# Performance work log

Hardware: AMD Instinct MI355X
Metric: run time of the kernel (lower is better)

The kernel has to match this reference:

```python
import jax, jax.numpy as jnp
import numpy as np

H = 50  # hidden_size


def _lstm_layer(x, W_ih, W_hh, b_ih, b_hh):
    """Single LSTM layer, batch_first input x: [B, T, D] -> [B, T, H].
    PyTorch gate order in the 4H dim: i, f, g, o."""
    B, T, D = x.shape
    # Precompute input projections for all timesteps: [T, B, 4H]
    x_proj = jnp.einsum('btd,gd->tbg', x, W_ih) + (b_ih + b_hh)

    def step(carry, xt):
        h, c = carry
        gates = xt + h @ W_hh.T  # [B, 4H]
        i, f, g, o = jnp.split(gates, 4, axis=-1)
        i = jax.nn.sigmoid(i)
        f = jax.nn.sigmoid(f)
        g = jnp.tanh(g)
        o = jax.nn.sigmoid(o)
        c = f * c + i * g
        h = o * jnp.tanh(c)
        return (h, c), h

    h0 = jnp.zeros((B, H), dtype=x.dtype)
    c0 = jnp.zeros((B, H), dtype=x.dtype)
    _, hs = jax.lax.scan(step, (h0, c0), x_proj)  # hs: [T, B, H]
    return jnp.transpose(hs, (1, 0, 2))  # [B, T, H]


def setup_inputs() -> dict:
    key = jax.random.key(0)
    ks = jax.random.split(key, 11)
    B, T = 2048, 512
    s = 1.0 / np.sqrt(H)  # PyTorch uniform init bound
    u = lambda k, shape: jax.random.uniform(k, shape, jnp.float32, -s, s)
    return {
        'x': jax.random.normal(ks[0], (B, T, 1), dtype=jnp.float32),
        'W_ih0': u(ks[1], (4 * H, 1)),
        'W_hh0': u(ks[2], (4 * H, H)),
        'b_ih0': u(ks[3], (4 * H,)),
        'b_hh0': u(ks[4], (4 * H,)),
        'W_ih1': u(ks[5], (4 * H, H)),
        'W_hh1': u(ks[6], (4 * H, H)),
        'b_ih1': u(ks[7], (4 * H,)),
        'b_hh1': u(ks[8], (4 * H,)),
        'W_fc': u(ks[9], (1, H)),
        'b_fc': u(ks[10], (1,)),
    }


def reference(x, W_ih0, W_hh0, b_ih0, b_hh0, W_ih1, W_hh1, b_ih1, b_hh1, W_fc, b_fc):
    out = _lstm_layer(x, W_ih0, W_hh0, b_ih0, b_hh0)     # [B, T, H]
    out = _lstm_layer(out, W_ih1, W_hh1, b_ih1, b_hh1)   # [B, T, H]
    return out[:, -1, :] @ W_fc.T + b_fc                  # [B, 1]
```

## Files before the change

### kernel.cpp

```cpp
#include <hip/hip_runtime.h>

#define TT   512
#define HH   50
#define MB   8
#define NW   13
#define NTHR (NW * 64)
#define BUFH 2560

typedef _Float16 f16x8 __attribute__((ext_vector_type(8)));
typedef float    f32x4 __attribute__((ext_vector_type(4)));

#define L2E 1.4426950408889634f

__device__ __forceinline__ float rcp_f(float v) { return __builtin_amdgcn_rcpf(v); }
__device__ __forceinline__ float ex2_f(float v) { return __builtin_amdgcn_exp2f(v); }

__global__ __launch_bounds__(NTHR, 1)
void lstm2_kernel(const float* __restrict__ x,
                  const float* __restrict__ W_ih0, const float* __restrict__ W_hh0,
                  const float* __restrict__ b_ih0, const float* __restrict__ b_hh0,
                  const float* __restrict__ W_ih1, const float* __restrict__ W_hh1,
                  const float* __restrict__ b_ih1, const float* __restrict__ b_hh1,
                  const float* __restrict__ W_fc,  const float* __restrict__ b_fc,
                  float* __restrict__ out)
{
    __shared__ __align__(16) _Float16 shh[2][BUFH];
    __shared__ float sh_x[MB][TT + 4];
    __shared__ float shf[MB][52];
    __shared__ float sh_wfc[HH];

    const int tid = threadIdx.x;
    const int w   = tid >> 6;
    const int l   = tid & 63;
    const int q   = l >> 4;
    const int n   = l & 15;
    const int b0  = blockIdx.x * MB;

    for (int i = tid; i < 2 * BUFH; i += NTHR) (&shh[0][0])[i] = (_Float16)0.0f;
    for (int i = tid; i < MB * TT; i += NTHR)
        sh_x[i >> 9][i & (TT - 1)] = x[(size_t)b0 * TT + i];
    for (int i = tid; i < HH; i += NTHR) sh_wfc[i] = W_fc[i];

    const int  u_r   = w * 4 + (n >> 2);
    const bool rowok = (u_r < HH);
    const int  grow  = (n & 3) * HH + (rowok ? u_r : 0);
    const float srow = ((n & 3) == 2) ? (2.0f * L2E) : (-L2E);

    f16x8 wf[5];
    #pragma unroll
    for (int ki = 0; ki < 5; ++ki) {
        #pragma unroll
        for (int e = 0; e < 8; ++e) {
            int k = ki * 32 + q * 8 + e;
            float v = 0.0f;
            if (rowok) {
                if      (k < HH)           v = W_hh0[grow * HH + k];
                else if (k < 2 * HH)       v = W_ih1[grow * HH + (k - HH)];
                else if (k < 3 * HH)       v = W_hh1[grow * HH + (k - 2 * HH)];
            }
            wf[ki][e] = (_Float16)(srow * v);
        }
    }

    const bool isL1 = (n >= 8);
    const int  u    = 4 * w + q;
    const int  cb   = n & 7;
    const bool wr   = (u < HH);
    const int  uc   = wr ? u : 0;

    float bz[4], wz[4];
    #pragma unroll
    for (int e = 0; e < 4; ++e) {
        int gr = e * HH + uc;
        float sc = (e == 2) ? (2.0f * L2E) : (-L2E);
        bz[e] = sc * (isL1 ? (b_ih1[gr] + b_hh1[gr]) : (b_ih0[gr] + b_hh0[gr]));
        wz[e] = isL1 ? 0.0f : (sc * W_ih0[gr]);
    }

    auto offrc = [](int r, int c) {
        return (r >> 5) * 512 + ((r >> 3) & 3) * 128 + c * 8 + (r & 7);
    };
    const _Float16* rb = &shh[0][8 * l];
    const int oa = isL1 ? offrc(100 + uc, cb + 8) : offrc(uc, cb);
    const int ob = offrc(50 + uc, cb + 8);
    _Float16* wpa0 = &shh[1][oa];
    _Float16* wpa1 = &shh[0][oa];
    _Float16* wpb0 = &shh[1][ob];
    _Float16* wpb1 = &shh[0][ob];

    const float* xq = &sh_x[cb][0];
    float cst = 0.0f;

    __syncthreads();

#define MFMA(A, B, C) __builtin_amdgcn_mfma_f32_16x16x32_f16((A), (B), (C), 0, 0, 0)

#define STEP(P, T0, XI)                                                           \
    {                                                                             \
        float xi = (XI);                                                          \
        f32x4 cin;                                                                \
        cin[0] = __builtin_fmaf(xi, wz[0], bz[0]);                                \
        cin[1] = __builtin_fmaf(xi, wz[1], bz[1]);                                \
        cin[2] = __builtin_fmaf(xi, wz[2], bz[2]);                                \
        cin[3] = __builtin_fmaf(xi, wz[3], bz[3]);                                \
        f16x8 b0 = *(const f16x8*)(rb + (P) * BUFH);                              \
        f16x8 b1 = *(const f16x8*)(rb + (P) * BUFH + 512);                        \
        f16x8 b2 = *(const f16x8*)(rb + (P) * BUFH + 1024);                       \
        f16x8 b3 = *(const f16x8*)(rb + (P) * BUFH + 1536);                       \
        f16x8 b4 = *(const f16x8*)(rb + (P) * BUFH + 2048);                       \
        f32x4 a = MFMA(wf[0], b0, cin);                                           \
        a = MFMA(wf[1], b1, a);                                                   \
        a = MFMA(wf[2], b2, a);                                                   \
        a = MFMA(wf[3], b3, a);                                                   \
        a = MFMA(wf[4], b4, a);                                                   \
        float eI = ex2_f(a[0]), eF = ex2_f(a[1]), tG = ex2_f(a[2]), eO = ex2_f(a[3]); \
        float dI = 1.0f + eI, dF = 1.0f + eF, dO = 1.0f + eO;                     \
        float IG = (tG - 1.0f) * rcp_f(dI * (tG + 1.0f));                         \
        float cn = __builtin_fmaf(rcp_f(dF), cst, IG);                            \
        cst = ((T0) && isL1) ? 0.0f : cn;                                         \
        float cc = __builtin_amdgcn_fmed3f(cst, -16.0f, 16.0f);                   \
        float tc = ex2_f(cc * (2.0f * L2E));                                      \
        float hv = (tc - 1.0f) * rcp_f(dO * (tc + 1.0f));                         \
        if (wr && !((T0) && isL1)) {                                              \
            _Float16 h16 = (_Float16)hv;                                          \
            *((P) ? wpa1 : wpa0) = h16;                                           \
            if (!isL1) *((P) ? wpb1 : wpb0) = h16;                                \
        }                                                                         \
        __syncthreads();                                                          \
    }

    STEP(0, 1, xq[0])
    for (int k2 = 0; k2 < 255; ++k2) {
        STEP(1, 0, xq[1])
        STEP(0, 0, xq[2])
        xq += 2;
    }
    STEP(1, 0, xq[1])
#undef STEP

    {
        f32x4 cin = {bz[0], bz[1], bz[2], bz[3]};
        f16x8 b0 = *(const f16x8*)(rb);
        f16x8 b1 = *(const f16x8*)(rb + 512);
        f16x8 b2 = *(const f16x8*)(rb + 1024);
        f16x8 b3 = *(const f16x8*)(rb + 1536);
        f16x8 b4 = *(const f16x8*)(rb + 2048);
        f32x4 a = MFMA(wf[0], b0, cin);
        a = MFMA(wf[1], b1, a);
        a = MFMA(wf[2], b2, a);
        a = MFMA(wf[3], b3, a);
        a = MFMA(wf[4], b4, a);
        if (isL1 && wr) {
            float eI = ex2_f(a[0]), eF = ex2_f(a[1]), tG = ex2_f(a[2]), eO = ex2_f(a[3]);
            float dI = 1.0f + eI, dF = 1.0f + eF, dO = 1.0f + eO;
            float IG = (tG - 1.0f) * rcp_f(dI * (tG + 1.0f));
            float cn = __builtin_fmaf(rcp_f(dF), cst, IG);
            float cc = __builtin_amdgcn_fmed3f(cn, -16.0f, 16.0f);
            float tc = ex2_f(cc * (2.0f * L2E));
            shf[cb][uc] = (tc - 1.0f) * rcp_f(dO * (tc + 1.0f));
        }
    }
    __syncthreads();

    if (tid < MB) {
        float s = b_fc[0];
        for (int j = 0; j < HH; ++j) s += shf[tid][j] * sh_wfc[j];
        out[b0 + tid] = s;
    }
#undef MFMA
}

extern "C" void kernel_launch(void* const* d_in, const int* in_sizes, int n_in,
                              void* d_out, int out_size, void* d_ws, size_t ws_size,
                              hipStream_t stream) {
    const float* xin   = (const float*)d_in[0];
    const float* W_ih0 = (const float*)d_in[1];
    const float* W_hh0 = (const float*)d_in[2];
    const float* b_ih0 = (const float*)d_in[3];
    const float* b_hh0 = (const float*)d_in[4];
    const float* W_ih1 = (const float*)d_in[5];
    const float* W_hh1 = (const float*)d_in[6];
    const float* b_ih1 = (const float*)d_in[7];
    const float* b_hh1 = (const float*)d_in[8];
    const float* W_fc  = (const float*)d_in[9];
    const float* b_fc  = (const float*)d_in[10];
    float* out = (float*)d_out;

    lstm2_kernel<<<dim3(2048 / MB), dim3(NTHR), 0, stream>>>(
        xin, W_ih0, W_hh0, b_ih0, b_hh0, W_ih1, W_hh1, b_ih1, b_hh1, W_fc, b_fc, out);
}
```

Before: 240.6 us.

## Halve wavefronts per block, each wave computing two hidden-unit tiles

Cuts the block from 13 wavefronts to 7, with each wave holding two sets of weight fragments and running two interleaved MFMA chains per timestep, covering 8 hidden units instead of 4. This makes the per-step __syncthreads cheaper and reuses the loaded B operands across two MFMA chains. Interleaving the two independent accumulation chains can hide MFMA latency. The cost is more register pressure and twice the gate math per wave on the serial critical path.

```diff
diff --git a/kernel.cpp b/kernel.cpp
--- a/kernel.cpp
+++ b/kernel.cpp
@@ -3,7 +3,7 @@
 #define TT   512
 #define HH   50
 #define MB   8
-#define NW   13
+#define NW   7
 #define NTHR (NW * 64)
 #define BUFH 2560
 
@@ -26,7 +26,7 @@
 {
     __shared__ __align__(16) _Float16 shh[2][BUFH];
     __shared__ float sh_x[MB][TT + 4];
-    __shared__ float shf[MB][52];
+    __shared__ float shf[MB][56];
     __shared__ float sh_wfc[HH];
 
     const int tid = threadIdx.x;
@@ -41,90 +41,122 @@
         sh_x[i >> 9][i & (TT - 1)] = x[(size_t)b0 * TT + i];
     for (int i = tid; i < HH; i += NTHR) sh_wfc[i] = W_fc[i];
 
-    const int  u_r   = w * 4 + (n >> 2);
-    const bool rowok = (u_r < HH);
-    const int  grow  = (n & 3) * HH + (rowok ? u_r : 0);
     const float srow = ((n & 3) == 2) ? (2.0f * L2E) : (-L2E);
-
-    f16x8 wf[5];
-    #pragma unroll
-    for (int ki = 0; ki < 5; ++ki) {
-        #pragma unroll
-        for (int e = 0; e < 8; ++e) {
-            int k = ki * 32 + q * 8 + e;
-            float v = 0.0f;
-            if (rowok) {
-                if      (k < HH)           v = W_hh0[grow * HH + k];
-                else if (k < 2 * HH)       v = W_ih1[grow * HH + (k - HH)];
-                else if (k < 3 * HH)       v = W_hh1[grow * HH + (k - 2 * HH)];
-            }
-            wf[ki][e] = (_Float16)(srow * v);
-        }
-    }
+    f16x8 wf0[5], wf1[5];
+
+#define LOADW(WF, TOFF)                                                           \
+    {                                                                             \
+        int ur   = 8 * w + (TOFF) + (n >> 2);                                     \
+        bool rok = (ur < HH);                                                     \
+        int grow = (n & 3) * HH + (rok ? ur : 0);                                 \
+        _Pragma("unroll")                                                         \
+        for (int ki = 0; ki < 5; ++ki) {                                          \
+            _Pragma("unroll")                                                     \
+            for (int e = 0; e < 8; ++e) {                                         \
+                int k = ki * 32 + q * 8 + e;                                      \
+                float v = 0.0f;                                                   \
+                if (rok) {                                                        \
+                    if      (k < HH)      v = W_hh0[grow * HH + k];               \
+                    else if (k < 2 * HH)  v = W_ih1[grow * HH + (k - HH)];        \
+                    else if (k < 3 * HH)  v = W_hh1[grow * HH + (k - 2 * HH)];    \
+                }                                                                 \
+                WF[ki][e] = (_Float16)(srow * v);                                 \
+            }                                                                     \
+        }                                                                         \
+    }
+    LOADW(wf0, 0)
+    LOADW(wf1, 4)
+#undef LOADW
 
     const bool isL1 = (n >= 8);
-    const int  u    = 4 * w + q;
     const int  cb   = n & 7;
-    const bool wr   = (u < HH);
-    const int  uc   = wr ? u : 0;
-
-    float bz[4], wz[4];
+    const int  u0   = 8 * w + q,      u1 = u0 + 4;
+    const bool wr0  = (u0 < HH),      wr1 = (u1 < HH);
+    const int  uc0  = wr0 ? u0 : 0;
+    const int  uc1  = wr1 ? u1 : 0;
+
+    float bz0[4], wz0[4], bz1[4], wz1[4];
     #pragma unroll
     for (int e = 0; e < 4; ++e) {
-        int gr = e * HH + uc;
         float sc = (e == 2) ? (2.0f * L2E) : (-L2E);
-        bz[e] = sc * (isL1 ? (b_ih1[gr] + b_hh1[gr]) : (b_ih0[gr] + b_hh0[gr]));
-        wz[e] = isL1 ? 0.0f : (sc * W_ih0[gr]);
+        int g0 = e * HH + uc0, g1 = e * HH + uc1;
+        bz0[e] = sc * (isL1 ? (b_ih1[g0] + b_hh1[g0]) : (b_ih0[g0] + b_hh0[g0]));
+        bz1[e] = sc * (isL1 ? (b_ih1[g1] + b_hh1[g1]) : (b_ih0[g1] + b_hh0[g1]));
+        wz0[e] = isL1 ? 0.0f : (sc * W_ih0[g0]);
+        wz1[e] = isL1 ? 0.0f : (sc * W_ih0[g1]);
     }
 
     auto offrc = [](int r, int c) {
         return (r >> 5) * 512 + ((r >> 3) & 3) * 128 + c * 8 + (r & 7);
     };
     const _Float16* rb = &shh[0][8 * l];
-    const int oa = isL1 ? offrc(100 + uc, cb + 8) : offrc(uc, cb);
-    const int ob = offrc(50 + uc, cb + 8);
-    _Float16* wpa0 = &shh[1][oa];
-    _Float16* wpa1 = &shh[0][oa];
-    _Float16* wpb0 = &shh[1][ob];
-    _Float16* wpb1 = &shh[0][ob];
+    const int oa0 = isL1 ? offrc(100 + uc0, cb + 8) : offrc(uc0, cb);
+    const int ob0 = offrc(50 + uc0, cb + 8);
+    const int oa1 = isL1 ? offrc(100 + uc1, cb + 8) : offrc(uc1, cb);
+    const int ob1 = offrc(50 + uc1, cb + 8);
 
     const float* xq = &sh_x[cb][0];
-    float cst = 0.0f;
+    float cst0 = 0.0f, cst1 = 0.0f;
 
     __syncthreads();
 
 #define MFMA(A, B, C) __builtin_amdgcn_mfma_f32_16x16x32_f16((A), (B), (C), 0, 0, 0)
+
+#define CHAIN(ACC, CST, T0, HV)                                                   \
+    {                                                                             \
+        float eI = ex2_f(ACC[0]), eF = ex2_f(ACC[1]);                             \
+        float tG = ex2_f(ACC[2]), eO = ex2_f(ACC[3]);                             \
+        float dI = 1.0f + eI, dF = 1.0f + eF, dO = 1.0f + eO;                     \
+        float IG = (tG - 1.0f) * rcp_f(dI * (tG + 1.0f));                         \
+        float cn = __builtin_fmaf(rcp_f(dF), CST, IG);                            \
+        CST = ((T0) && isL1) ? 0.0f : cn;                                         \
+        float cc = __builtin_amdgcn_fmed3f(CST, -16.0f, 16.0f);                   \
+        float tc = ex2_f(cc * (2.0f * L2E));                                      \
+        HV = (tc - 1.0f) * rcp_f(dO * (tc + 1.0f));                               \
+    }
 
 #define STEP(P, T0, XI)                                                           \
     {                                                                             \
         float xi = (XI);                                                          \
-        f32x4 cin;                                                                \
-        cin[0] = __builtin_fmaf(xi, wz[0], bz[0]);                                \
-        cin[1] = __builtin_fmaf(xi, wz[1], bz[1]);                                \
-        cin[2] = __builtin_fmaf(xi, wz[2], bz[2]);                                \
-        cin[3] = __builtin_fmaf(xi, wz[3], bz[3]);                                \
+        f32x4 cin0, cin1;                                                         \
+        cin0[0] = __builtin_fmaf(xi, wz0[0], bz0[0]);                             \
+        cin0[1] = __builtin_fmaf(xi, wz0[1], bz0[1]);                             \
+        cin0[2] = __builtin_fmaf(xi, wz0[2], bz0[2]);                             \
+        cin0[3] = __builtin_fmaf(xi, wz0[3], bz0[3]);                             \
+        cin1[0] = __builtin_fmaf(xi, wz1[0], bz1[0]);                             \
+        cin1[1] = __builtin_fmaf(xi, wz1[1], bz1[1]);                             \
+        cin1[2] = __builtin_fmaf(xi, wz1[2], bz1[2]);                             \
+        cin1[3] = __builtin_fmaf(xi, wz1[3], bz1[3]);                             \
         f16x8 b0 = *(const f16x8*)(rb + (P) * BUFH);                              \
         f16x8 b1 = *(const f16x8*)(rb + (P) * BUFH + 512);                        \
         f16x8 b2 = *(const f16x8*)(rb + (P) * BUFH + 1024);                       \
         f16x8 b3 = *(const f16x8*)(rb + (P) * BUFH + 1536);                       \
         f16x8 b4 = *(const f16x8*)(rb + (P) * BUFH + 2048);                       \
-        f32x4 a = MFMA(wf[0], b0, cin);                                           \
-        a = MFMA(wf[1], b1, a);                                                   \
-        a = MFMA(wf[2], b2, a);                                                   \
-        a = MFMA(wf[3], b3, a);                                                   \
-        a = MFMA(wf[4], b4, a);                                                   \
-        float eI = ex2_f(a[0]), eF = ex2_f(a[1]), tG = ex2_f(a[2]), eO = ex2_f(a[3]); \
-        float dI = 1.0f + eI, dF = 1.0f + eF, dO = 1.0f + eO;                     \
-        float IG = (tG - 1.0f) * rcp_f(dI * (tG + 1.0f));                         \
-        float cn = __builtin_fmaf(rcp_f(dF), cst, IG);                            \
-        cst = ((T0) && isL1) ? 0.0f : cn;                                         \
-        float cc = __builtin_amdgcn_fmed3f(cst, -16.0f, 16.0f);                   \
-        float tc = ex2_f(cc * (2.0f * L2E));                                      \
-        float hv = (tc - 1.0f) * rcp_f(dO * (tc + 1.0f));                         \
-        if (wr && !((T0) && isL1)) {                                              \
-            _Float16 h16 = (_Float16)hv;                                          \
-            *((P) ? wpa1 : wpa0) = h16;                                           \
-            if (!isL1) *((P) ? wpb1 : wpb0) = h16;                                \
+        f32x4 a0 = MFMA(wf0[0], b0, cin0);                                        \
+        f32x4 a1 = MFMA(wf1[0], b0, cin1);                                        \
+        a0 = MFMA(wf0[1], b1, a0);                                                \
+        a1 = MFMA(wf1[1], b1, a1);                                                \
+        a0 = MFMA(wf0[2], b2, a0);                                                \
+        a1 = MFMA(wf1[2], b2, a1);                                                \
+        a0 = MFMA(wf0[3], b3, a0);                                                \
+        a1 = MFMA(wf1[3], b3, a1);                                                \
+        a0 = MFMA(wf0[4], b4, a0);                                                \
+        a1 = MFMA(wf1[4], b4, a1);                                                \
+        float hv0, hv1;                                                           \
+        CHAIN(a0, cst0, T0, hv0)                                                  \
+        CHAIN(a1, cst1, T0, hv1)                                                  \
+        if (!((T0) && isL1)) {                                                    \
+            _Float16* wbuf = &shh[(P) ^ 1][0];                                    \
+            if (wr0) {                                                            \
+                _Float16 h16 = (_Float16)hv0;                                     \
+                wbuf[oa0] = h16;                                                  \
+                if (!isL1) wbuf[ob0] = h16;                                       \
+            }                                                                     \
+            if (wr1) {                                                            \
+                _Float16 h16 = (_Float16)hv1;                                     \
+                wbuf[oa1] = h16;                                                  \
+                if (!isL1) wbuf[ob1] = h16;                                       \
+            }                                                                     \
         }                                                                         \
         __syncthreads();                                                          \
     }
@@ -139,25 +171,29 @@
 #undef STEP
 
     {
-        f32x4 cin = {bz[0], bz[1], bz[2], bz[3]};
+        f32x4 cin0 = {bz0[0], bz0[1], bz0[2], bz0[3]};
+        f32x4 cin1 = {bz1[0], bz1[1], bz1[2], bz1[3]};
         f16x8 b0 = *(const f16x8*)(rb);
         f16x8 b1 = *(const f16x8*)(rb + 512);
         f16x8 b2 = *(const f16x8*)(rb + 1024);
         f16x8 b3 = *(const f16x8*)(rb + 1536);
         f16x8 b4 = *(const f16x8*)(rb + 2048);
-        f32x4 a = MFMA(wf[0], b0, cin);
-        a = MFMA(wf[1], b1, a);
-        a = MFMA(wf[2], b2, a);
-        a = MFMA(wf[3], b3, a);
-        a = MFMA(wf[4], b4, a);
-        if (isL1 && wr) {
-            float eI = ex2_f(a[0]), eF = ex2_f(a[1]), tG = ex2_f(a[2]), eO = ex2_f(a[3]);
-            float dI = 1.0f + eI, dF = 1.0f + eF, dO = 1.0f + eO;
-            float IG = (tG - 1.0f) * rcp_f(dI * (tG + 1.0f));
-            float cn = __builtin_fmaf(rcp_f(dF), cst, IG);
-            float cc = __builtin_amdgcn_fmed3f(cn, -16.0f, 16.0f);
-            float tc = ex2_f(cc * (2.0f * L2E));
-            shf[cb][uc] = (tc - 1.0f) * rcp_f(dO * (tc + 1.0f));
+        f32x4 a0 = MFMA(wf0[0], b0, cin0);
+        f32x4 a1 = MFMA(wf1[0], b0, cin1);
+        a0 = MFMA(wf0[1], b1, a0);
+        a1 = MFMA(wf1[1], b1, a1);
+        a0 = MFMA(wf0[2], b2, a0);
+        a1 = MFMA(wf1[2], b2, a1);
+        a0 = MFMA(wf0[3], b3, a0);
+        a1 = MFMA(wf1[3], b3, a1);
+        a0 = MFMA(wf0[4], b4, a0);
+        a1 = MFMA(wf1[4], b4, a1);
+        if (isL1) {
+            float hv0, hv1;
+            CHAIN(a0, cst0, 0, hv0)
+            CHAIN(a1, cst1, 0, hv1)
+            if (wr0) shf[cb][uc0] = hv0;
+            if (wr1) shf[cb][uc1] = hv1;
         }
     }
     __syncthreads();
@@ -167,6 +203,7 @@
         for (int j = 0; j < HH; ++j) s += shf[tid][j] * sh_wfc[j];
         out[b0 + tid] = s;
     }
+#undef CHAIN
 #undef MFMA
 }
 
```

New measurement: 269.4 us. +11.9%, slower.
